# Optimization experiments

Hardware: AMD Instinct MI355X
Metric: run time of the kernel (lower is better)

The kernel has to match this reference:

```python
import jax, jax.numpy as jnp
import numpy as np

N = 100_000       # nodes
E = 1_600_000     # edges (avg degree 16)
F_IN = 10         # num_node_features
H = 128           # hidden_dim
L = 3             # num_layers
G = 256           # number of graphs in the batch
C = 25            # num_classes
BN_EPS = 1e-5


def setup_inputs() -> dict:
    key = jax.random.key(0)
    ks = jax.random.split(key, 10)
    s = 0.05
    x = jax.random.normal(ks[0], (N, F_IN), dtype=jnp.float32)
    edge_index = jax.random.randint(ks[1], (2, E), 0, N, dtype=jnp.int32)
    batch = jnp.sort(jax.random.randint(ks[2], (N,), 0, G, dtype=jnp.int32))
    return {
        "x": x,
        "edge_index": edge_index,
        "batch": batch,
        "Wp": jax.random.normal(ks[3], (F_IN, H), dtype=jnp.float32) * s,
        "bp": jnp.zeros((H,), jnp.float32),
        "Wc": jax.random.normal(ks[4], (L, H, H), dtype=jnp.float32) * s,
        "bc": jnp.zeros((L, H), jnp.float32),
        "bn_gamma": jnp.ones((L, H), jnp.float32),
        "bn_beta": jnp.zeros((L, H), jnp.float32),
        "bn_mean": jax.random.normal(ks[5], (L, H), dtype=jnp.float32) * 0.1,
        "bn_var": jax.random.uniform(ks[6], (L, H), minval=0.5, maxval=1.5, dtype=jnp.float32),
        "W1": jax.random.normal(ks[7], (2 * H, H), dtype=jnp.float32) * s,
        "b1": jnp.zeros((H,), jnp.float32),
        "W2": jax.random.normal(ks[8], (H, C), dtype=jnp.float32) * s,
        "b2": jnp.zeros((C,), jnp.float32),
    }


def reference(x, edge_index, batch, Wp, bp, Wc, bc, bn_gamma, bn_beta,
              bn_mean, bn_var, W1, b1, W2, b2):
    n = x.shape[0]
    # GCNConv: add self loops, symmetric degree normalization (eval semantics:
    # batchnorm uses running stats, dropout is identity).
    loop = jnp.arange(n, dtype=edge_index.dtype)
    rows = jnp.concatenate([edge_index[0], loop])  # target / aggregation index
    cols = jnp.concatenate([edge_index[1], loop])  # source / gather index
    deg = jax.ops.segment_sum(jnp.ones_like(rows, dtype=x.dtype), rows, num_segments=n)
    dinv = jax.lax.rsqrt(deg)  # deg >= 1 thanks to self loops
    norm = dinv[rows] * dinv[cols]  # [E+N]

    h = jax.nn.relu(x @ Wp + bp)
    for i in range(L):
        hw = h @ Wc[i]                                   # [N, H]
        msg = hw[cols] * norm[:, None]                   # gather + scale
        agg = jax.ops.segment_sum(msg, rows, num_segments=n) + bc[i]
        bn = (agg - bn_mean[i]) * jax.lax.rsqrt(bn_var[i] + BN_EPS) * bn_gamma[i] + bn_beta[i]
        h = jax.nn.relu(bn)

    counts = jax.ops.segment_sum(jnp.ones((n,), h.dtype), batch, num_segments=G)
    x_mean = jax.ops.segment_sum(h, batch, num_segments=G) / jnp.maximum(counts, 1.0)[:, None]
    x_max = jax.ops.segment_max(h, batch, num_segments=G)
    x_max = jnp.where(counts[:, None] > 0, x_max, 0.0)   # guard empty graphs
    g = jnp.concatenate([x_mean, x_max], axis=1)          # [G, 2H]
    return jax.nn.relu(g @ W1 + b1) @ W2 + b2             # [G, C]
```

## Files before the change

### kernel.cpp

```cpp
#include <hip/hip_runtime.h>

#define N_NODES   100000
#define N_EDGES   1600000
#define F_IN      10
#define HD        128
#define N_LAYERS  3
#define N_GRAPHS  256
#define N_CLASSES 25
#define BN_EPS    1e-5f
#define POOL_TILE 64
#define LDS_PITCH 152
#define CPITCH    136

#define NBUCK     196
#define SCAT_TILE 4096
#define BCAP      9216
#define BUCK_CAP  16384
#define PREPW_BLKS ((N_LAYERS*HD*HD)/256)
#define PROJ_BLKS 1024

typedef __attribute__((ext_vector_type(8))) short bf8;
typedef __attribute__((ext_vector_type(4))) float f32x4;

static __device__ __forceinline__ unsigned short f2bf(float f){
    unsigned u = __float_as_uint(f);
    unsigned r = (u + 0x7fffu + ((u >> 16) & 1u)) >> 16;
    return (unsigned short)r;
}
static __device__ __forceinline__ float bflo(unsigned u){ return __uint_as_float(u << 16); }
static __device__ __forceinline__ float bfhi(unsigned u){ return __uint_as_float(u & 0xffff0000u); }
static __device__ __forceinline__ unsigned packbf(float a, float b){
    return (unsigned)f2bf(a) | ((unsigned)f2bf(b) << 16);
}

__global__ __launch_bounds__(256) void k_scatter(const int* __restrict__ rows,
        const int* __restrict__ cols, int* __restrict__ gcur,
        unsigned* __restrict__ ebuf, int e, int nsb,
        const float* __restrict__ Wc, unsigned short* __restrict__ WT,
        const float* __restrict__ x, const float* __restrict__ Wp,
        const float* __restrict__ bp, unsigned* __restrict__ hbf, int n){
    __shared__ int lbase[NBUCK];
    __shared__ int lcur[NBUCK];
    __shared__ int gbase[NBUCK];
    __shared__ int sbuf[256];
    __shared__ unsigned sedge[SCAT_TILE];
    __shared__ unsigned char sbuck[SCAT_TILE];
    __shared__ float sW[F_IN*HD];
    __shared__ float sb[HD];
    int t = threadIdx.x;

    if (blockIdx.x >= nsb){
        int bid2 = blockIdx.x - nsb;
        if (bid2 < PREPW_BLKS){
            int i = bid2*256 + t;
            int l = i >> 14;
            int r = (i >> 7) & 127;
            int c = i & 127;
            WT[(l << 14) + c*HD + r] = f2bf(Wc[i]);
            return;
        }
        int bid = bid2 - PREPW_BLKS;
        for (int q = t; q < F_IN*HD; q += 256) sW[q] = Wp[q];
        if (t < HD) sb[t] = bp[t];
        __syncthreads();
        int j  = t & 63;
        int ln = t >> 6;
        for (int n0 = bid*4 + ln; n0 < n; n0 += PROJ_BLKS*4){
            float a0 = sb[2*j], a1 = sb[2*j+1];
            #pragma unroll
            for (int k = 0; k < F_IN; k++){
                float xv = x[(size_t)n0*F_IN + k];
                a0 += xv * sW[k*HD + 2*j];
                a1 += xv * sW[k*HD + 2*j+1];
            }
            hbf[(size_t)n0*64 + j] = packbf(fmaxf(a0, 0.f), fmaxf(a1, 0.f));
        }
        return;
    }

    int i0 = blockIdx.x*SCAT_TILE + t;
    int r[16], c[16];
    if (t < NBUCK) lcur[t] = 0;
    __syncthreads();
    #pragma unroll
    for (int k = 0; k < 16; k++){
        int i = i0 + k*256;
        if (i < e){
            r[k] = rows[i]; c[k] = cols[i];
            atomicAdd(&lcur[r[k] >> 9], 1);
        } else r[k] = -1;
    }
    __syncthreads();
    int myc = (t < NBUCK) ? lcur[t] : 0;
    sbuf[t] = myc;
    __syncthreads();
    for (int d = 1; d < 256; d <<= 1){
        int tv = (t >= d) ? sbuf[t-d] : 0;
        __syncthreads();
        sbuf[t] += tv;
        __syncthreads();
    }
    if (t < NBUCK){
        lbase[t] = sbuf[t] - myc;
        lcur[t]  = sbuf[t] - myc;
        if (myc > 0) gbase[t] = t*BCAP + atomicAdd(&gcur[t], myc);
    }
    __syncthreads();
    #pragma unroll
    for (int k = 0; k < 16; k++){
        if (r[k] >= 0){
            int bk = r[k] >> 9;
            int off = atomicAdd(&lcur[bk], 1);
            sedge[off] = ((unsigned)(r[k] & 511) << 17) | (unsigned)c[k];
            sbuck[off] = (unsigned char)bk;
        }
    }
    __syncthreads();
    int tot = sbuf[255];
    for (int i = t; i < tot; i += 256){
        int bk = sbuck[i];
        ebuf[gbase[bk] + (i - lbase[bk])] = sedge[i];
    }
}

__global__ __launch_bounds__(512) void k_build(const unsigned* __restrict__ ebuf,
        const int* __restrict__ gcur, int* __restrict__ rowptr,
        float* __restrict__ dinv, int* __restrict__ colidx, int n, int etot){
    __shared__ int hist[512];
    __shared__ int cur[512];
    __shared__ int colstage[BUCK_CAP];
    __shared__ int sscan[256];
    int t = threadIdx.x;
    int gval = (t < NBUCK) ? gcur[t] : 0;
    if (t < 256) sscan[t] = gval;
    __syncthreads();
    for (int d = 1; d < 256; d <<= 1){
        int tv = (t < 256 && t >= d) ? sscan[t-d] : 0;
        __syncthreads();
        if (t < 256) sscan[t] += tv;
        __syncthreads();
    }
    int b = blockIdx.x;
    int cnt = gcur[b];
    int s   = sscan[b] - cnt;
    int sp  = b*BCAP;
    int row0 = b << 9;
    int nrows = min(512, n - row0);
    if (b == 0 && t == 0) rowptr[n] = etot;
    hist[t] = 0;
    __syncthreads();
    for (int i = t; i < cnt; i += 512)
        atomicAdd(&hist[ebuf[sp + i] >> 17], 1);
    __syncthreads();
    int myc = hist[t];
    cur[t] = myc;
    __syncthreads();
    for (int d = 1; d < 512; d <<= 1){
        int tv = (t >= d) ? cur[t-d] : 0;
        __syncthreads();
        cur[t] += tv;
        __syncthreads();
    }
    int excl = cur[t] - myc;
    if (t < nrows){
        rowptr[row0 + t] = s + excl;
        dinv[row0 + t] = rsqrtf((float)(myc + 1));
    }
    cur[t] = excl;
    __syncthreads();
    for (int i = t; i < cnt; i += 512){
        unsigned v = ebuf[sp + i];
        int off = atomicAdd(&cur[v >> 17], 1);
        colstage[off] = (int)(v & 0x1ffffu);
    }
    __syncthreads();
    for (int i = t; i < cnt; i += 512)
        colidx[s + i] = colstage[i];
}

__global__ __launch_bounds__(512) void k_gemm(const unsigned short* __restrict__ hbf,
        const unsigned short* __restrict__ WT, const float* __restrict__ dinv,
        unsigned short* __restrict__ hw, int n){
    extern __shared__ char smem[];
    unsigned short* As = (unsigned short*)smem;
    unsigned short* Bs = As + 128*LDS_PITCH;
    int tid = threadIdx.x;
    int row0 = blockIdx.x * 128;

    const uint4* h4 = (const uint4*)hbf;
    const uint4* w4 = (const uint4*)WT;
    #pragma unroll
    for (int q = tid; q < 2048; q += 512){
        int r = q >> 4, c = q & 15;
        uint4 v = make_uint4(0u,0u,0u,0u);
        if (row0 + r < n) v = h4[(size_t)(row0 + r)*16 + c];
        *(uint4*)&As[r*LDS_PITCH + c*8] = v;
        *(uint4*)&Bs[r*LDS_PITCH + c*8] = w4[r*16 + c];
    }
    __syncthreads();

    int w = tid >> 6, lane = tid & 63;
    int l15 = lane & 15, quad = lane >> 4;
    f32x4 acc[8];
    #pragma unroll
    for (int ct = 0; ct < 8; ct++) acc[ct] = (f32x4){0.f,0.f,0.f,0.f};

    int arow = w*16 + l15;
    #pragma unroll
    for (int kc = 0; kc < 4; kc++){
        int ko = kc*32 + quad*8;
        bf8 a = *(const bf8*)&As[arow*LDS_PITCH + ko];
        #pragma unroll
        for (int ct = 0; ct < 8; ct++){
            bf8 b = *(const bf8*)&Bs[(ct*16 + l15)*LDS_PITCH + ko];
            acc[ct] = __builtin_amdgcn_mfma_f32_16x16x32_bf16(a, b, acc[ct], 0, 0, 0);
        }
    }
    __syncthreads();

    unsigned short* CS = As;
    #pragma unroll
    for (int reg = 0; reg < 4; reg++){
        int rloc = w*16 + quad*4 + reg;
        int grow = row0 + rloc;
        float dv = (grow < n) ? dinv[grow] : 0.f;
        #pragma unroll
        for (int ct = 0; ct < 8; ct++)
            CS[rloc*CPITCH + ct*16 + l15] = f2bf(acc[ct][reg] * dv);
    }
    __syncthreads();

    #pragma unroll
    for (int q = tid; q < 2048; q += 512){
        int r = q >> 4, c = q & 15;
        if (row0 + r < n)
            *(uint4*)&hw[(size_t)(row0 + r)*HD + c*8] = *(const uint4*)&CS[r*CPITCH + c*8];
    }
}

__global__ __launch_bounds__(256) void k_agg(const uint4* __restrict__ hw4,
        const int* __restrict__ rowptr, const int* __restrict__ colidx,
        const float* __restrict__ dinv, const float* __restrict__ bc,
        const float* __restrict__ bmean, const float* __restrict__ bvar,
        const float* __restrict__ bgamma, const float* __restrict__ bbeta,
        uint4* __restrict__ houtb, int n){
    int lane = threadIdx.x & 63;
    int grp  = lane >> 4;
    int fl   = lane & 15;
    int node = blockIdx.x*16 + (threadIdx.x >> 6)*4 + grp;
    bool valid = node < n;
    int nd = valid ? node : 0;

    float a[8], b[8];
    uint4 self = hw4[(size_t)nd*16 + fl];
    a[0] = bflo(self.x); a[1] = bfhi(self.x);
    a[2] = bflo(self.y); a[3] = bfhi(self.y);
    a[4] = bflo(self.z); a[5] = bfhi(self.z);
    a[6] = bflo(self.w); a[7] = bfhi(self.w);
    #pragma unroll
    for (int j = 0; j < 8; j++) b[j] = 0.f;

    int s = rowptr[nd];
    int e = valid ? rowptr[nd+1] : s;
    int t = s;

    #define ACC(dst, v) { dst[0]+=bflo(v.x); dst[1]+=bfhi(v.x); \
                          dst[2]+=bflo(v.y); dst[3]+=bfhi(v.y); \
                          dst[4]+=bflo(v.z); dst[5]+=bfhi(v.z); \
                          dst[6]+=bflo(v.w); dst[7]+=bfhi(v.w); }

    for (; t + 8 <= e; t += 8){
        int c0 = colidx[t],   c1 = colidx[t+1];
        int c2 = colidx[t+2], c3 = colidx[t+3];
        int c4 = colidx[t+4], c5 = colidx[t+5];
        int c6 = colidx[t+6], c7 = colidx[t+7];
        uint4 v0 = hw4[(size_t)c0*16 + fl];
        uint4 v1 = hw4[(size_t)c1*16 + fl];
        uint4 v2 = hw4[(size_t)c2*16 + fl];
        uint4 v3 = hw4[(size_t)c3*16 + fl];
        uint4 v4 = hw4[(size_t)c4*16 + fl];
        uint4 v5 = hw4[(size_t)c5*16 + fl];
        uint4 v6 = hw4[(size_t)c6*16 + fl];
        uint4 v7 = hw4[(size_t)c7*16 + fl];
        ACC(a, v0); ACC(b, v1); ACC(a, v2); ACC(b, v3);
        ACC(a, v4); ACC(b, v5); ACC(a, v6); ACC(b, v7);
    }
    for (; t + 4 <= e; t += 4){
        int c0 = colidx[t],   c1 = colidx[t+1];
        int c2 = colidx[t+2], c3 = colidx[t+3];
        uint4 v0 = hw4[(size_t)c0*16 + fl];
        uint4 v1 = hw4[(size_t)c1*16 + fl];
        uint4 v2 = hw4[(size_t)c2*16 + fl];
        uint4 v3 = hw4[(size_t)c3*16 + fl];
        ACC(a, v0); ACC(b, v1); ACC(a, v2); ACC(b, v3);
    }
    for (; t < e; t++){
        uint4 v = hw4[(size_t)colidx[t]*16 + fl];
        ACC(a, v);
    }
    #undef ACC
    #pragma unroll
    for (int j = 0; j < 8; j++) a[j] += b[j];

    if (!valid) return;
    float dv = dinv[node];
    const float4* B4 = (const float4*)bc;
    const float4* M4 = (const float4*)bmean;
    const float4* V4 = (const float4*)bvar;
    const float4* G4 = (const float4*)bgamma;
    const float4* T4 = (const float4*)bbeta;
    float4 cb[2] = {B4[fl*2], B4[fl*2+1]};
    float4 cm[2] = {M4[fl*2], M4[fl*2+1]};
    float4 cv[2] = {V4[fl*2], V4[fl*2+1]};
    float4 cg[2] = {G4[fl*2], G4[fl*2+1]};
    float4 ct[2] = {T4[fl*2], T4[fl*2+1]};
    float r[8];
    #pragma unroll
    for (int j = 0; j < 8; j++){
        float cbj = ((const float*)cb)[j];
        float cmj = ((const float*)cm)[j];
        float cvj = ((const float*)cv)[j];
        float cgj = ((const float*)cg)[j];
        float ctj = ((const float*)ct)[j];
        float rx = (a[j]*dv + cbj - cmj) * rsqrtf(cvj + BN_EPS) * cgj + ctj;
        r[j] = fmaxf(rx, 0.f);
    }
    uint4 o;
    o.x = packbf(r[0], r[1]);
    o.y = packbf(r[2], r[3]);
    o.z = packbf(r[4], r[5]);
    o.w = packbf(r[6], r[7]);
    houtb[(size_t)node*16 + fl] = o;
}

__global__ void k_pool(const unsigned* __restrict__ hb, const int* __restrict__ batch,
        float* __restrict__ gsum, int* __restrict__ gmax, int n){
    int q = threadIdx.x;
    int start = blockIdx.x * POOL_TILE;
    int end = min(start + POOL_TILE, n);
    if (start >= end) return;
    int cur = batch[start];
    float s0 = 0.f, s1 = 0.f, m0 = 0.f, m1 = 0.f;
    for (int i = start; i < end; i++){
        int b = batch[i];
        unsigned v = hb[(size_t)i*64 + q];
        float v0 = bflo(v), v1 = bfhi(v);
        if (b != cur){
            atomicAdd(&gsum[cur*HD + 2*q],     s0);
            atomicAdd(&gsum[cur*HD + 2*q + 1], s1);
            atomicMax(&gmax[cur*HD + 2*q],     __float_as_int(m0));
            atomicMax(&gmax[cur*HD + 2*q + 1], __float_as_int(m1));
            s0 = s1 = m0 = m1 = 0.f; cur = b;
        }
        s0 += v0; s1 += v1;
        m0 = fmaxf(m0, v0); m1 = fmaxf(m1, v1);
    }
    atomicAdd(&gsum[cur*HD + 2*q],     s0);
    atomicAdd(&gsum[cur*HD + 2*q + 1], s1);
    atomicMax(&gmax[cur*HD + 2*q],     __float_as_int(m0));
    atomicMax(&gmax[cur*HD + 2*q + 1], __float_as_int(m1));
}

__global__ void k_head(const float* __restrict__ gsum, const int* __restrict__ gmax,
        const int* __restrict__ batch, const float* __restrict__ W1,
        const float* __restrict__ b1, const float* __restrict__ W2,
        const float* __restrict__ b2, float* __restrict__ out, int n){
    __shared__ float gv[2*HD];
    __shared__ float hid[HD];
    __shared__ int bound[2];
    int g = blockIdx.x, j = threadIdx.x;
    if (j < 2){
        int target = g + j;
        int lo = 0, hi = n;
        while (lo < hi){ int mid = (lo + hi) >> 1; if (batch[mid] < target) lo = mid + 1; else hi = mid; }
        bound[j] = lo;
    }
    __syncthreads();
    float denom = (float)max(bound[1] - bound[0], 1);
    gv[j]    = gsum[g*HD+j] / denom;
    gv[HD+j] = __int_as_float(gmax[g*HD+j]);
    __syncthreads();
    float acc = b1[j];
    #pragma unroll 8
    for (int k = 0; k < 2*HD; k++) acc += gv[k]*W1[k*HD + j];
    hid[j] = fmaxf(acc, 0.f);
    __syncthreads();
    if (j < N_CLASSES){
        float o = b2[j];
        #pragma unroll 4
        for (int k = 0; k < HD; k++) o += hid[k]*W2[k*N_CLASSES + j];
        out[g*N_CLASSES + j] = o;
    }
}

extern "C" void kernel_launch(void* const* d_in, const int* in_sizes, int n_in,
                              void* d_out, int out_size, void* d_ws, size_t ws_size,
                              hipStream_t stream){
    const float* x   = (const float*)d_in[0];
    const int*  eidx = (const int*)d_in[1];
    const int* batch = (const int*)d_in[2];
    const float* Wp  = (const float*)d_in[3];
    const float* bp  = (const float*)d_in[4];
    const float* Wc  = (const float*)d_in[5];
    const float* bc  = (const float*)d_in[6];
    const float* bng = (const float*)d_in[7];
    const float* bnb = (const float*)d_in[8];
    const float* bnm = (const float*)d_in[9];
    const float* bnv = (const float*)d_in[10];
    const float* W1  = (const float*)d_in[11];
    const float* b1  = (const float*)d_in[12];
    const float* W2  = (const float*)d_in[13];
    const float* b2  = (const float*)d_in[14];
    float* out = (float*)d_out;

    char* ws = (char*)d_ws;
    size_t off = 0;
    unsigned short* h_bf  = (unsigned short*)(ws + off); off += (size_t)N_NODES*HD*2;
    unsigned short* hw_bf = (unsigned short*)(ws + off); off += (size_t)N_NODES*HD*2;
    unsigned short* WT = (unsigned short*)(ws + off); off += (size_t)N_LAYERS*HD*HD*2;
    float* dinv   = (float*)(ws + off); off += (size_t)N_NODES*4;
    int*   rowptr = (int*)  (ws + off); off += (size_t)(N_NODES+16)*4;
    int*   colidx = (int*)  (ws + off); off += (size_t)N_EDGES*4;
    unsigned* ebuf= (unsigned*)(ws + off); off += (size_t)NBUCK*BCAP*4;
    int*   gcur   = (int*)  (ws + off); off += 1024;
    float* gsum   = (float*)(ws + off); off += (size_t)N_GRAPHS*HD*4;
    int*   gmax   = (int*)  (ws + off); off += (size_t)N_GRAPHS*HD*4;

    const int* rows = eidx;
    const int* cols = eidx + N_EDGES;

    hipMemsetAsync(gcur, 0, 1024 + (size_t)(N_GRAPHS*HD*2)*4, stream);

    int nsb = (N_EDGES + SCAT_TILE - 1)/SCAT_TILE;
    k_scatter<<<nsb + PREPW_BLKS + PROJ_BLKS, 256, 0, stream>>>(rows, cols, gcur, ebuf,
        N_EDGES, nsb, Wc, WT, x, Wp, bp, (unsigned*)h_bf, N_NODES);
    k_build  <<<NBUCK, 512, 0, stream>>>(ebuf, gcur, rowptr, dinv, colidx, N_NODES, N_EDGES);

    int ntiles = (N_NODES + 127)/128;
    size_t shmem = (size_t)(2*128*LDS_PITCH)*2;
    for (int l = 0; l < N_LAYERS; l++){
        k_gemm<<<ntiles, 512, shmem, stream>>>(h_bf, WT + (size_t)l*HD*HD, dinv, hw_bf, N_NODES);
        k_agg<<<(N_NODES+15)/16, 256, 0, stream>>>((const uint4*)hw_bf, rowptr, colidx, dinv,
            bc + l*HD, bnm + l*HD, bnv + l*HD, bng + l*HD, bnb + l*HD,
            (uint4*)h_bf, N_NODES);
    }

    k_pool<<<(N_NODES+POOL_TILE-1)/POOL_TILE, 64, 0, stream>>>((const unsigned*)h_bf, batch, gsum, gmax, N_NODES);
    k_head<<<N_GRAPHS, 128, 0, stream>>>(gsum, gmax, batch, W1, b1, W2, b2, out, N_NODES);
}
```

Measured before the change: 408.6 us.

## Split node features into column slices so gathers stay cache-resident per slice

Node feature buffers change from row-major [N,128] bf16 to eight feature slices of 16 columns each, stored slice-major. The aggregation kernel now processes one slice per block for 128 nodes, with two threads per node, and stages rowptr and column indices in LDS. Each slice (about 3.2 MB) can fit in L2, so the random neighbor gathers should hit cache instead of DRAM. The cost is that column indices are reread eight times and each node gets less parallelism per thread; the GEMM and pooling kernels are adjusted to the new layout.

```diff
diff --git a/kernel.cpp b/kernel.cpp
--- a/kernel.cpp
+++ b/kernel.cpp
@@ -18,6 +18,12 @@
 #define BUCK_CAP  16384
 #define PREPW_BLKS ((N_LAYERS*HD*HD)/256)
 #define PROJ_BLKS 1024
+
+#define AGG_ND    128
+#define AGG_ECAP  4096
+
+#define SLICE_U4  ((size_t)N_NODES*2)
+#define SLICE_U1  ((size_t)N_NODES*8)
 
 typedef __attribute__((ext_vector_type(8))) short bf8;
 typedef __attribute__((ext_vector_type(4))) float f32x4;
@@ -65,6 +71,7 @@
         __syncthreads();
         int j  = t & 63;
         int ln = t >> 6;
+        size_t sbase = (size_t)(j >> 3)*SLICE_U1 + (j & 7);
         for (int n0 = bid*4 + ln; n0 < n; n0 += PROJ_BLKS*4){
             float a0 = sb[2*j], a1 = sb[2*j+1];
             #pragma unroll
@@ -73,7 +80,7 @@
                 a0 += xv * sW[k*HD + 2*j];
                 a1 += xv * sW[k*HD + 2*j+1];
             }
-            hbf[(size_t)n0*64 + j] = packbf(fmaxf(a0, 0.f), fmaxf(a1, 0.f));
+            hbf[sbase + (size_t)n0*8] = packbf(fmaxf(a0, 0.f), fmaxf(a1, 0.f));
         }
         return;
     }
@@ -178,23 +185,31 @@
         colidx[s + i] = colstage[i];
 }
 
-__global__ __launch_bounds__(512) void k_gemm(const unsigned short* __restrict__ hbf,
+__global__ __launch_bounds__(512) void k_gemm(const uint4* __restrict__ h4,
         const unsigned short* __restrict__ WT, const float* __restrict__ dinv,
-        unsigned short* __restrict__ hw, int n){
+        uint4* __restrict__ hw, int n){
     extern __shared__ char smem[];
     unsigned short* As = (unsigned short*)smem;
     unsigned short* Bs = As + 128*LDS_PITCH;
     int tid = threadIdx.x;
     int row0 = blockIdx.x * 128;
 
-    const uint4* h4 = (const uint4*)hbf;
     const uint4* w4 = (const uint4*)WT;
+    #pragma unroll
+    for (int q = tid; q < 1024; q += 512){
+        int r = q & 127, sc = q >> 7;
+        int grow = row0 + r;
+        uint4 v0 = make_uint4(0u,0u,0u,0u), v1 = v0;
+        if (grow < n){
+            size_t bidx = (size_t)sc*SLICE_U4 + (size_t)grow*2;
+            v0 = h4[bidx]; v1 = h4[bidx + 1];
+        }
+        *(uint4*)&As[r*LDS_PITCH + sc*16]     = v0;
+        *(uint4*)&As[r*LDS_PITCH + sc*16 + 8] = v1;
+    }
     #pragma unroll
     for (int q = tid; q < 2048; q += 512){
         int r = q >> 4, c = q & 15;
-        uint4 v = make_uint4(0u,0u,0u,0u);
-        if (row0 + r < n) v = h4[(size_t)(row0 + r)*16 + c];
-        *(uint4*)&As[r*LDS_PITCH + c*8] = v;
         *(uint4*)&Bs[r*LDS_PITCH + c*8] = w4[r*16 + c];
     }
     __syncthreads();
@@ -231,10 +246,14 @@
     __syncthreads();
 
     #pragma unroll
-    for (int q = tid; q < 2048; q += 512){
-        int r = q >> 4, c = q & 15;
-        if (row0 + r < n)
-            *(uint4*)&hw[(size_t)(row0 + r)*HD + c*8] = *(const uint4*)&CS[r*CPITCH + c*8];
+    for (int q = tid; q < 1024; q += 512){
+        int r = q & 127, sc = q >> 7;
+        int grow = row0 + r;
+        if (grow < n){
+            size_t bidx = (size_t)sc*SLICE_U4 + (size_t)grow*2;
+            hw[bidx]     = *(const uint4*)&CS[r*CPITCH + sc*16];
+            hw[bidx + 1] = *(const uint4*)&CS[r*CPITCH + sc*16 + 8];
+        }
     }
 }
 
@@ -244,15 +263,32 @@
         const float* __restrict__ bmean, const float* __restrict__ bvar,
         const float* __restrict__ bgamma, const float* __restrict__ bbeta,
         uint4* __restrict__ houtb, int n){
-    int lane = threadIdx.x & 63;
-    int grp  = lane >> 4;
-    int fl   = lane & 15;
-    int node = blockIdx.x*16 + (threadIdx.x >> 6)*4 + grp;
-    bool valid = node < n;
-    int nd = valid ? node : 0;
+    __shared__ int scol[AGG_ECAP];
+    __shared__ int srp[AGG_ND + 1];
+    int tid = threadIdx.x;
+    int slice = blockIdx.x & 7;
+    int chunk = blockIdx.x >> 3;
+    int n0 = chunk * AGG_ND;
+    int nloc = min(AGG_ND, n - n0);
+
+    for (int i = tid; i <= nloc; i += 256) srp[i] = rowptr[n0 + i];
+    __syncthreads();
+    int ebase = srp[0];
+    int ecnt  = srp[nloc] - ebase;
+    bool inl = (ecnt <= AGG_ECAP);
+    if (inl){
+        for (int i = tid; i < ecnt; i += 256) scol[i] = colidx[ebase + i];
+    }
+    __syncthreads();
+    const int* col = inl ? (const int*)scol : (colidx + ebase);
+
+    int nd = tid >> 1, hf = tid & 1;
+    bool valid = nd < nloc;
+    int node = n0 + (valid ? nd : 0);
+    const uint4* base = hw4 + (size_t)slice*SLICE_U4;
 
     float a[8], b[8];
-    uint4 self = hw4[(size_t)nd*16 + fl];
+    uint4 self = base[(size_t)node*2 + hf];
     a[0] = bflo(self.x); a[1] = bfhi(self.x);
     a[2] = bflo(self.y); a[3] = bfhi(self.y);
     a[4] = bflo(self.z); a[5] = bfhi(self.z);
@@ -260,8 +296,8 @@
     #pragma unroll
     for (int j = 0; j < 8; j++) b[j] = 0.f;
 
-    int s = rowptr[nd];
-    int e = valid ? rowptr[nd+1] : s;
+    int s = valid ? (srp[nd]   - ebase) : 0;
+    int e = valid ? (srp[nd+1] - ebase) : 0;
     int t = s;
 
     #define ACC(dst, v) { dst[0]+=bflo(v.x); dst[1]+=bfhi(v.x); \
@@ -270,32 +306,32 @@
                           dst[6]+=bflo(v.w); dst[7]+=bfhi(v.w); }
 
     for (; t + 8 <= e; t += 8){
-        int c0 = colidx[t],   c1 = colidx[t+1];
-        int c2 = colidx[t+2], c3 = colidx[t+3];
-        int c4 = colidx[t+4], c5 = colidx[t+5];
-        int c6 = colidx[t+6], c7 = colidx[t+7];
-        uint4 v0 = hw4[(size_t)c0*16 + fl];
-        uint4 v1 = hw4[(size_t)c1*16 + fl];
-        uint4 v2 = hw4[(size_t)c2*16 + fl];
-        uint4 v3 = hw4[(size_t)c3*16 + fl];
-        uint4 v4 = hw4[(size_t)c4*16 + fl];
-        uint4 v5 = hw4[(size_t)c5*16 + fl];
-        uint4 v6 = hw4[(size_t)c6*16 + fl];
-        uint4 v7 = hw4[(size_t)c7*16 + fl];
+        int c0 = col[t],   c1 = col[t+1];
+        int c2 = col[t+2], c3 = col[t+3];
+        int c4 = col[t+4], c5 = col[t+5];
+        int c6 = col[t+6], c7 = col[t+7];
+        uint4 v0 = base[(size_t)c0*2 + hf];
+        uint4 v1 = base[(size_t)c1*2 + hf];
+        uint4 v2 = base[(size_t)c2*2 + hf];
+        uint4 v3 = base[(size_t)c3*2 + hf];
+        uint4 v4 = base[(size_t)c4*2 + hf];
+        uint4 v5 = base[(size_t)c5*2 + hf];
+        uint4 v6 = base[(size_t)c6*2 + hf];
+        uint4 v7 = base[(size_t)c7*2 + hf];
         ACC(a, v0); ACC(b, v1); ACC(a, v2); ACC(b, v3);
         ACC(a, v4); ACC(b, v5); ACC(a, v6); ACC(b, v7);
     }
     for (; t + 4 <= e; t += 4){
-        int c0 = colidx[t],   c1 = colidx[t+1];
-        int c2 = colidx[t+2], c3 = colidx[t+3];
-        uint4 v0 = hw4[(size_t)c0*16 + fl];
-        uint4 v1 = hw4[(size_t)c1*16 + fl];
-        uint4 v2 = hw4[(size_t)c2*16 + fl];
-        uint4 v3 = hw4[(size_t)c3*16 + fl];
+        int c0 = col[t],   c1 = col[t+1];
+        int c2 = col[t+2], c3 = col[t+3];
+        uint4 v0 = base[(size_t)c0*2 + hf];
+        uint4 v1 = base[(size_t)c1*2 + hf];
+        uint4 v2 = base[(size_t)c2*2 + hf];
+        uint4 v3 = base[(size_t)c3*2 + hf];
         ACC(a, v0); ACC(b, v1); ACC(a, v2); ACC(b, v3);
     }
     for (; t < e; t++){
-        uint4 v = hw4[(size_t)colidx[t]*16 + fl];
+        uint4 v = base[(size_t)col[t]*2 + hf];
         ACC(a, v);
     }
     #undef ACC
@@ -304,25 +340,17 @@
 
     if (!valid) return;
     float dv = dinv[node];
-    const float4* B4 = (const float4*)bc;
-    const float4* M4 = (const float4*)bmean;
-    const float4* V4 = (const float4*)bvar;
-    const float4* G4 = (const float4*)bgamma;
-    const float4* T4 = (const float4*)bbeta;
-    float4 cb[2] = {B4[fl*2], B4[fl*2+1]};
-    float4 cm[2] = {M4[fl*2], M4[fl*2+1]};
-    float4 cv[2] = {V4[fl*2], V4[fl*2+1]};
-    float4 cg[2] = {G4[fl*2], G4[fl*2+1]};
-    float4 ct[2] = {T4[fl*2], T4[fl*2+1]};
+    int f4 = slice*4 + hf*2;
+    float cb[8], cm[8], cv[8], cg[8], ct[8];
+    *(float4*)&cb[0] = ((const float4*)bc)[f4];     *(float4*)&cb[4] = ((const float4*)bc)[f4+1];
+    *(float4*)&cm[0] = ((const float4*)bmean)[f4];  *(float4*)&cm[4] = ((const float4*)bmean)[f4+1];
+    *(float4*)&cv[0] = ((const float4*)bvar)[f4];   *(float4*)&cv[4] = ((const float4*)bvar)[f4+1];
+    *(float4*)&cg[0] = ((const float4*)bgamma)[f4]; *(float4*)&cg[4] = ((const float4*)bgamma)[f4+1];
+    *(float4*)&ct[0] = ((const float4*)bbeta)[f4];  *(float4*)&ct[4] = ((const float4*)bbeta)[f4+1];
     float r[8];
     #pragma unroll
     for (int j = 0; j < 8; j++){
-        float cbj = ((const float*)cb)[j];
-        float cmj = ((const float*)cm)[j];
-        float cvj = ((const float*)cv)[j];
-        float cgj = ((const float*)cg)[j];
-        float ctj = ((const float*)ct)[j];
-        float rx = (a[j]*dv + cbj - cmj) * rsqrtf(cvj + BN_EPS) * cgj + ctj;
+        float rx = (a[j]*dv + cb[j] - cm[j]) * rsqrtf(cv[j] + BN_EPS) * cg[j] + ct[j];
         r[j] = fmaxf(rx, 0.f);
     }
     uint4 o;
@@ -330,7 +358,7 @@
     o.y = packbf(r[2], r[3]);
     o.z = packbf(r[4], r[5]);
     o.w = packbf(r[6], r[7]);
-    houtb[(size_t)node*16 + fl] = o;
+    houtb[(size_t)slice*SLICE_U4 + (size_t)node*2 + hf] = o;
 }
 
 __global__ void k_pool(const unsigned* __restrict__ hb, const int* __restrict__ batch,
@@ -339,11 +367,12 @@
     int start = blockIdx.x * POOL_TILE;
     int end = min(start + POOL_TILE, n);
     if (start >= end) return;
+    size_t sbase = (size_t)(q >> 3)*SLICE_U1 + (q & 7);
     int cur = batch[start];
     float s0 = 0.f, s1 = 0.f, m0 = 0.f, m1 = 0.f;
     for (int i = start; i < end; i++){
         int b = batch[i];
-        unsigned v = hb[(size_t)i*64 + q];
+        unsigned v = hb[sbase + (size_t)i*8];
         float v0 = bflo(v), v1 = bfhi(v);
         if (b != cur){
             atomicAdd(&gsum[cur*HD + 2*q],     s0);
@@ -437,10 +466,12 @@
     k_build  <<<NBUCK, 512, 0, stream>>>(ebuf, gcur, rowptr, dinv, colidx, N_NODES, N_EDGES);
 
     int ntiles = (N_NODES + 127)/128;
+    int aggblk = ((N_NODES + AGG_ND - 1)/AGG_ND) * 8;
     size_t shmem = (size_t)(2*128*LDS_PITCH)*2;
     for (int l = 0; l < N_LAYERS; l++){
-        k_gemm<<<ntiles, 512, shmem, stream>>>(h_bf, WT + (size_t)l*HD*HD, dinv, hw_bf, N_NODES);
-        k_agg<<<(N_NODES+15)/16, 256, 0, stream>>>((const uint4*)hw_bf, rowptr, colidx, dinv,
+        k_gemm<<<ntiles, 512, shmem, stream>>>((const uint4*)h_bf, WT + (size_t)l*HD*HD, dinv,
+            (uint4*)hw_bf, N_NODES);
+        k_agg<<<aggblk, 256, 0, stream>>>((const uint4*)hw_bf, rowptr, colidx, dinv,
             bc + l*HD, bnm + l*HD, bnv + l*HD, bng + l*HD, bnb + l*HD,
             (uint4*)h_bf, N_NODES);
     }
```

Result: slower. 443.6 us (+8.6%).
